# Kernel optimization log

Measured on AMD Instinct MI355X. Metric: run time of the kernel, lower is better.

The kernel has to match this reference:

```python
import jax, jax.numpy as jnp
import numpy as np
from jax import lax

B, C_IN, C_OUT, KK, KS = 8, 32, 64, 4, 3
D, H, W = 32, 64, 64
PAD = 1

def setup_inputs() -> dict:
    key = jax.random.key(0)
    ks = jax.random.split(key, 12)
    s = 0.02
    return {
        "x": jax.random.normal(ks[0], (B, C_IN, D, H, W), jnp.float32),
        # K candidate conv kernels and biases
        "weight": jax.random.normal(ks[1], (KK, C_OUT, C_IN, KS, KS, KS), jnp.float32) * s,
        "cbias": jnp.zeros((KK, C_OUT), jnp.float32),
        "temperature": jnp.float32(34.0),
        # attention key path: BN(affine, eval-mode) -> GELU -> 1x1 conv (linear)
        "bn1_g": jnp.ones((C_IN,), jnp.float32),
        "bn1_b": jnp.zeros((C_IN,), jnp.float32),
        "w1": jax.random.normal(ks[2], (C_IN, C_IN), jnp.float32) * s,
        "b1": jnp.zeros((C_IN,), jnp.float32),
        "bn2_g": jnp.ones((C_IN,), jnp.float32),
        "bn2_b": jnp.zeros((C_IN,), jnp.float32),
        "w2": jax.random.normal(ks[3], (C_IN, C_IN), jnp.float32) * s,
        "b2": jnp.zeros((C_IN,), jnp.float32),
        "bn3_g": jnp.ones((C_IN,), jnp.float32),
        "bn3_b": jnp.zeros((C_IN,), jnp.float32),
        "w3": jax.random.normal(ks[4], (KK, C_IN), jnp.float32) * s,
        "b3": jnp.zeros((KK,), jnp.float32),
    }

def _attention(p, temperature, bn1_g, bn1_b, w1, b1, bn2_g, bn2_b, w2, b2, bn3_g, bn3_b, w3, b3):
    # p: [B, C] pooled features. 1x1x1 convs on 1x1x1 maps == linear layers.
    gelu = lambda t: jax.nn.gelu(t, approximate=False)  # torch nn.GELU default is erf
    a = gelu(p * bn1_g + bn1_b)          # BN (eval: rm=0, rv=1) + GELU
    a = a @ w1.T + b1
    a = gelu(a * bn2_g + bn2_b)
    a = a @ w2.T + b2
    a = a + p                            # ResidualLayer (plain add)
    a = a * bn3_g + bn3_b
    logits = a @ w3.T + b3               # [B, K]
    return jax.nn.softmax(logits / temperature, axis=1)

def reference(x, weight, cbias, temperature, bn1_g, bn1_b, w1, b1,
              bn2_g, bn2_b, w2, b2, bn3_g, bn3_b, w3, b3):
    # x: [B, C_in, D, H, W]
    p = x.mean(axis=(2, 3, 4))  # AdaptiveAvgPool3d(1)
    attn = _attention(p, temperature, bn1_g, bn1_b, w1, b1,
                      bn2_g, bn2_b, w2, b2, bn3_g, bn3_b, w3, b3)  # [B, K]
    # per-sample aggregated kernels / bias
    agg_w = jnp.einsum('bk,koidhw->boidhw', attn, weight)  # [B, O, I, k, k, k]
    agg_b = attn @ cbias                                    # [B, O]
    # grouped-conv trick (groups=B) == per-sample conv3d -> vmap over batch
    def conv1(xi, wi):
        return lax.conv_general_dilated(
            xi[None], wi, window_strides=(1, 1, 1),
            padding=[(PAD, PAD)] * 3,
            dimension_numbers=('NCDHW', 'OIDHW', 'NCDHW'))[0]
    out = jax.vmap(conv1)(x, agg_w)  # [B, O, D, H, W]
    return out + agg_b[:, :, None, None, None]
```

## Files before the change

### kernel.cpp

```cpp
#include <hip/hip_runtime.h>
#include <hip/hip_bf16.h>
#include <math.h>

#define B_   8
#define CIN  32
#define COUT 64
#define KK_  4
#define DD   32
#define HH   64
#define WW   64
#define HW   (HH*WW)
#define DHW  (DD*HH*WW)

typedef __attribute__((ext_vector_type(8)))  short bf16x8;
typedef __attribute__((ext_vector_type(16))) float f32x16;

__device__ __forceinline__ unsigned short f2bf(float f) {
    union { float f; unsigned int u; } v; v.f = f;
    return (unsigned short)((v.u + 0x7FFFu + ((v.u >> 16) & 1u)) >> 16);
}
__device__ __forceinline__ void gll16(const void* g, void* l) {
    __builtin_amdgcn_global_load_lds(
        (const __attribute__((address_space(1))) void*)g,
        (__attribute__((address_space(3))) void*)l, 16, 0, 0);
}

__global__ __launch_bounds__(256) void transpose_kernel(const float* __restrict__ x,
                                                        unsigned short* __restrict__ xt,
                                                        float* __restrict__ pblk) {
    const int t = threadIdx.x;
    const int r = t >> 6, w = t & 63;
    const int hb = blockIdx.x;
    const int h = (hb << 2) + r;
    const int d = blockIdx.y, b = blockIdx.z;

    const float* xb = x + (size_t)b*CIN*DHW + (size_t)d*HW + (size_t)h*WW + w;
    float f[CIN];
    #pragma unroll
    for (int c = 0; c < CIN; ++c) f[c] = xb[(size_t)c * DHW];

    unsigned int packed[CIN/2];
    #pragma unroll
    for (int c2 = 0; c2 < CIN/2; ++c2) {
        unsigned int lo = f2bf(f[2*c2]);
        unsigned int hi = f2bf(f[2*c2+1]);
        packed[c2] = lo | (hi << 16);
    }
    char* row = (char*)xt + (size_t)((b*DD + d)*HH + h) * 4096;
    #pragma unroll
    for (int q = 0; q < 4; ++q) {
        uint4 v = make_uint4(packed[4*q], packed[4*q+1], packed[4*q+2], packed[4*q+3]);
        *(uint4*)(row + q*1024 + (((w << 4)) ^ (q << 4))) = v;
    }

    #pragma unroll
    for (int off = 32; off > 0; off >>= 1) {
        #pragma unroll
        for (int c = 0; c < CIN; ++c) f[c] += __shfl_xor(f[c], off);
    }
    __shared__ float ws4[4][CIN];
    if ((t & 63) < CIN) ws4[r][t & 63] = f[t & 63];
    __syncthreads();
    if (t < CIN)
        pblk[(size_t)((b*DD + d)*16 + hb)*CIN + t] =
            ws4[0][t] + ws4[1][t] + ws4[2][t] + ws4[3][t];
}

__device__ __forceinline__ float gelu_erf(float v) {
    return 0.5f * v * (1.f + erff(v * 0.70710678118654752f));
}

__global__ void attn_kernel(const float* __restrict__ pblk,
                            const float* __restrict__ temperature,
                            const float* __restrict__ bn1_g, const float* __restrict__ bn1_b,
                            const float* __restrict__ w1,    const float* __restrict__ b1,
                            const float* __restrict__ bn2_g, const float* __restrict__ bn2_b,
                            const float* __restrict__ w2,    const float* __restrict__ b2,
                            const float* __restrict__ bn3_g, const float* __restrict__ bn3_b,
                            const float* __restrict__ w3,    const float* __restrict__ b3,
                            const float* __restrict__ cbias,
                            float* __restrict__ attn_out, float* __restrict__ aggb_out) {
    __shared__ float A[B_][CIN], A2[B_][CIN];
    __shared__ float L[B_][KK_], ATT[B_][KK_];
    const int t = threadIdx.x;
    const int b = t >> 5, c = t & 31;

    float pv = 0.f;
    for (int i = 0; i < DD*16; ++i) pv += pblk[(size_t)(b*DD*16 + i)*CIN + c];
    pv *= (1.f / (float)DHW);

    A[b][c] = gelu_erf(pv * bn1_g[c] + bn1_b[c]);
    __syncthreads();

    float s = b1[c];
    for (int j = 0; j < CIN; ++j) s += A[b][j] * w1[c*CIN + j];
    A2[b][c] = gelu_erf(s * bn2_g[c] + bn2_b[c]);
    __syncthreads();

    float s2 = b2[c];
    for (int j = 0; j < CIN; ++j) s2 += A2[b][j] * w2[c*CIN + j];
    s2 += pv;
    s2 = s2 * bn3_g[c] + bn3_b[c];
    __syncthreads();
    A[b][c] = s2;
    __syncthreads();

    if (c < KK_) {
        float lv = b3[c];
        for (int j = 0; j < CIN; ++j) lv += A[b][j] * w3[c*CIN + j];
        L[b][c] = lv;
    }
    __syncthreads();

    const float T = temperature[0];
    if (c < KK_) {
        float m = fmaxf(fmaxf(L[b][0], L[b][1]), fmaxf(L[b][2], L[b][3]));
        float e = expf((L[b][c] - m) / T);
        float den = 0.f;
        for (int j = 0; j < KK_; ++j) den += expf((L[b][j] - m) / T);
        float av = e / den;
        ATT[b][c] = av;
        attn_out[b*KK_ + c] = av;
    }
    __syncthreads();

    for (int o = c; o < COUT; o += CIN) {
        float sb = 0.f;
        for (int k = 0; k < KK_; ++k) sb += ATT[b][k] * cbias[k*COUT + o];
        aggb_out[b*COUT + o] = sb;
    }
}

__global__ void aggw_kernel(const float* __restrict__ weight,
                            const float* __restrict__ attn,
                            unsigned short* __restrict__ wt) {
    const int idx = blockIdx.x * 256 + threadIdx.x;
    const int ci   = idx & 31;
    const int co   = (idx >> 5) & 63;
    int r          = idx >> 11;
    const int kpos = r % 27;
    const int b    = r / 27;
    float s = 0.f;
    #pragma unroll
    for (int k = 0; k < KK_; ++k)
        s += attn[b*KK_ + k] * weight[((k*COUT + co)*CIN + ci)*27 + kpos];
    wt[idx] = f2bf(s);
}

__global__ __launch_bounds__(128, 1) void conv_mfma(const unsigned short* __restrict__ xt,
                                                    const unsigned short* __restrict__ wt,
                                                    const float* __restrict__ aggb,
                                                    float* __restrict__ out) {
    __shared__ char smem[19 * 4096];
    const int t    = threadIdx.x;
    const int lane = t & 63;
    const int wv   = t >> 6;
    const int lw   = lane & 31, lh = lane >> 5;

    const int id = blockIdx.x;
    const int b  = id & 7;
    const int cv = (id >> 3) & 1;
    const int h  = (id >> 4) & 63;
    const int d0 = ((id >> 10) & 7) << 2;

    const char* xb  = (const char*)xt + (size_t)(b*DD)*HH*4096;
    const char* wtb = (const char*)wt + (size_t)b * 27 * 4096 + (cv << 11);

    *(uint4*)&smem[18*4096 + t*32]      = make_uint4(0u,0u,0u,0u);
    *(uint4*)&smem[18*4096 + t*32 + 16] = make_uint4(0u,0u,0u,0u);

    for (int rid = wv; rid < 18; rid += 2) {
        const int j = rid / 3, ho = rid % 3;
        const int zd = d0 - 1 + j, yh = h - 1 + ho;
        char* dst = smem + (size_t)(rid << 12);
        if ((unsigned)zd < DD && (unsigned)yh < HH) {
            const char* src = xb + (size_t)(zd*HH + yh)*4096 + lane*16;
            #pragma unroll
            for (int q = 0; q < 4; ++q) gll16(src + (q << 10), dst + (q << 10));
        } else {
            #pragma unroll
            for (int q = 0; q < 4; ++q)
                *(uint4*)(dst + (q << 10) + lane*16) = make_uint4(0u,0u,0u,0u);
        }
    }

    const int a_off = lw*64 + lh*16;
    bf16x8 avv[27][2];
    #pragma unroll
    for (int kp = 0; kp < 27; ++kp) {
        const char* wk = wtb + (size_t)(kp << 12);
        avv[kp][0] = *(const bf16x8*)(wk + a_off);
        avv[kp][1] = *(const bf16x8*)(wk + 32 + a_off);
    }

    __syncthreads();

    f32x16 acc[4];
    #pragma unroll
    for (int r = 0; r < 4; ++r) acc[r] = (f32x16){};

    const int o0 = lh, o1 = 2 + lh;

    bf16x8 bcp[2][12];
    auto loadB = [&](int p, int par) {
        const int kh = p / 3, kw = p % 3;
        const int wp  = (wv << 5) + lw + kw - 1;
        const bool oob = ((unsigned)wp >= (unsigned)WW);
        const int wpc = oob ? lw : wp;
        const int sw0 = (o0 << 10) + ((wpc << 4) ^ (o0 << 4));
        const int sw1 = (o1 << 10) + ((wpc << 4) ^ (o1 << 4));
        #pragma unroll
        for (int j = 0; j < 6; ++j) {
            const int rb = oob ? 18*4096 : ((j*3 + kh) << 12);
            bcp[par][j*2+0] = *(const bf16x8*)&smem[rb + sw0];
            bcp[par][j*2+1] = *(const bf16x8*)&smem[rb + sw1];
        }
    };

    loadB(0, 0);

    #pragma unroll
    for (int p = 0; p < 9; ++p) {
        const int cur = p & 1, nxt = cur ^ 1;
        if (p < 8) loadB(p + 1, nxt);
        __builtin_amdgcn_sched_barrier(0);
        const int kh = p / 3, kw = p % 3;
        __builtin_amdgcn_s_setprio(1);
        #pragma unroll
        for (int kd = 0; kd < 3; ++kd) {
            const int kp = (kd*3 + kh)*3 + kw;
            #pragma unroll
            for (int r = 0; r < 4; ++r) {
                const int j = r + kd;
                acc[r] = __builtin_amdgcn_mfma_f32_32x32x16_bf16(avv[kp][0], bcp[cur][j*2+0], acc[r], 0, 0, 0);
                acc[r] = __builtin_amdgcn_mfma_f32_32x32x16_bf16(avv[kp][1], bcp[cur][j*2+1], acc[r], 0, 0, 0);
            }
        }
        __builtin_amdgcn_s_setprio(0);
    }

    const float* ab = aggb + b*COUT;
    const int sp0 = h*WW + (wv << 5) + lw;
    #pragma unroll
    for (int reg = 0; reg < 16; ++reg) {
        const int co = (cv << 5) + (reg & 3) + ((reg >> 2) << 3) + (lh << 2);
        const float bb = ab[co];
        float* oc = out + ((size_t)(b*COUT + co))*DHW + sp0;
        #pragma unroll
        for (int r = 0; r < 4; ++r)
            oc[(size_t)(d0 + r)*HW] = acc[r][reg] + bb;
    }
}

extern "C" void kernel_launch(void* const* d_in, const int* in_sizes, int n_in,
                              void* d_out, int out_size, void* d_ws, size_t ws_size,
                              hipStream_t stream) {
    const float* x           = (const float*)d_in[0];
    const float* weight      = (const float*)d_in[1];
    const float* cbias       = (const float*)d_in[2];
    const float* temperature = (const float*)d_in[3];
    const float* bn1_g       = (const float*)d_in[4];
    const float* bn1_b       = (const float*)d_in[5];
    const float* w1          = (const float*)d_in[6];
    const float* b1          = (const float*)d_in[7];
    const float* bn2_g       = (const float*)d_in[8];
    const float* bn2_b       = (const float*)d_in[9];
    const float* w2          = (const float*)d_in[10];
    const float* b2          = (const float*)d_in[11];
    const float* bn3_g       = (const float*)d_in[12];
    const float* bn3_b       = (const float*)d_in[13];
    const float* w3          = (const float*)d_in[14];
    const float* b3          = (const float*)d_in[15];
    float* out = (float*)d_out;

    char* ws = (char*)d_ws;
    float*          attn = (float*)(ws + 1024);
    float*          aggb = (float*)(ws + 4096);
    float*          pblk = (float*)(ws + 65536);
    unsigned short* wt   = (unsigned short*)(ws + 622592);
    unsigned short* xt   = (unsigned short*)(ws + 1507328);

    transpose_kernel<<<dim3(HH/4, DD, B_), 256, 0, stream>>>(x, xt, pblk);
    attn_kernel<<<1, 256, 0, stream>>>(pblk, temperature,
                                       bn1_g, bn1_b, w1, b1,
                                       bn2_g, bn2_b, w2, b2,
                                       bn3_g, bn3_b, w3, b3,
                                       cbias, attn, aggb);
    aggw_kernel<<<(B_*27*COUT*CIN)/256, 256, 0, stream>>>(weight, attn, wt);
    conv_mfma<<<dim3(8192), 128, 0, stream>>>(xt, wt, aggb, out);
}
```

Baseline: 216.5 us.

## Make conv blocks loop over depth with a ring-buffered, prefetched LDS slab pipeline

The conv kernel now launches one 256-thread block per (batch, row), 512 blocks in total. Each block's four waves split the output channels and the width between them, and the block walks all 32 depth planes in steps of four. Input slabs live in a 10-slot LDS ring: the slabs for the next step are prefetched with global_load_lds while the current step runs MFMAs. Weights stay in registers for the whole depth loop, and the bias is folded into the accumulator init. This removes the repeated halo loads and per-block weight reloads of the old 8192-block launch. The cost is less parallelism, and the barrier's vmcnt(63) wait may not guarantee the prefetched slabs have landed before they are read.

```diff
diff --git a/kernel.cpp b/kernel.cpp
--- a/kernel.cpp
+++ b/kernel.cpp
@@ -147,42 +147,24 @@
     wt[idx] = f2bf(s);
 }
 
-__global__ __launch_bounds__(128, 1) void conv_mfma(const unsigned short* __restrict__ xt,
+__global__ __launch_bounds__(256, 1) void conv_mfma(const unsigned short* __restrict__ xt,
                                                     const unsigned short* __restrict__ wt,
                                                     const float* __restrict__ aggb,
                                                     float* __restrict__ out) {
-    __shared__ char smem[19 * 4096];
+    __shared__ char smem[126976];
     const int t    = threadIdx.x;
     const int lane = t & 63;
-    const int wv   = t >> 6;
+    const int wid  = t >> 6;
+    const int cv   = wid >> 1;
+    const int wv   = wid & 1;
     const int lw   = lane & 31, lh = lane >> 5;
 
     const int id = blockIdx.x;
     const int b  = id & 7;
-    const int cv = (id >> 3) & 1;
-    const int h  = (id >> 4) & 63;
-    const int d0 = ((id >> 10) & 7) << 2;
+    const int h  = id >> 3;
 
     const char* xb  = (const char*)xt + (size_t)(b*DD)*HH*4096;
     const char* wtb = (const char*)wt + (size_t)b * 27 * 4096 + (cv << 11);
-
-    *(uint4*)&smem[18*4096 + t*32]      = make_uint4(0u,0u,0u,0u);
-    *(uint4*)&smem[18*4096 + t*32 + 16] = make_uint4(0u,0u,0u,0u);
-
-    for (int rid = wv; rid < 18; rid += 2) {
-        const int j = rid / 3, ho = rid % 3;
-        const int zd = d0 - 1 + j, yh = h - 1 + ho;
-        char* dst = smem + (size_t)(rid << 12);
-        if ((unsigned)zd < DD && (unsigned)yh < HH) {
-            const char* src = xb + (size_t)(zd*HH + yh)*4096 + lane*16;
-            #pragma unroll
-            for (int q = 0; q < 4; ++q) gll16(src + (q << 10), dst + (q << 10));
-        } else {
-            #pragma unroll
-            for (int q = 0; q < 4; ++q)
-                *(uint4*)(dst + (q << 10) + lane*16) = make_uint4(0u,0u,0u,0u);
-        }
-    }
 
     const int a_off = lw*64 + lh*16;
     bf16x8 avv[27][2];
@@ -192,63 +174,108 @@
         avv[kp][0] = *(const bf16x8*)(wk + a_off);
         avv[kp][1] = *(const bf16x8*)(wk + 32 + a_off);
     }
-
+    #pragma unroll
+    for (int kp = 0; kp < 27; ++kp) {
+        asm volatile("" : "+v"(avv[kp][0]));
+        asm volatile("" : "+v"(avv[kp][1]));
+    }
+
+    f32x16 binit;
+    #pragma unroll
+    for (int reg = 0; reg < 16; ++reg)
+        binit[reg] = aggb[b*COUT + (cv << 5) + (reg & 3) + ((reg >> 2) << 3) + (lh << 2)];
+
+    *(uint4*)&smem[122880 + t*16] = make_uint4(0u,0u,0u,0u);
+
+    auto stage_slab = [&](int zd, int slot) {
+        char* sb = smem + slot * 12288;
+        #pragma unroll
+        for (int ho = 0; ho < 3; ++ho) {
+            const int yh = h - 1 + ho;
+            char* dst = sb + (ho << 12);
+            if ((unsigned)zd < DD && (unsigned)yh < HH) {
+                const char* src = xb + ((size_t)(zd*HH + yh) << 12) + lane*16;
+                #pragma unroll
+                for (int q = 0; q < 4; ++q) gll16(src + (q << 10), dst + (q << 10));
+            } else {
+                #pragma unroll
+                for (int q = 0; q < 4; ++q)
+                    *(uint4*)(dst + (q << 10) + lane*16) = make_uint4(0u,0u,0u,0u);
+            }
+        }
+    };
+
+    for (int i = wid; i < 6; i += 4) stage_slab(i - 1, (i + 9) % 10);
     __syncthreads();
 
     f32x16 acc[4];
     #pragma unroll
-    for (int r = 0; r < 4; ++r) acc[r] = (f32x16){};
+    for (int r = 0; r < 4; ++r) acc[r] = binit;
 
     const int o0 = lh, o1 = 2 + lh;
-
+    const int ZR = 122880;
     bf16x8 bcp[2][12];
-    auto loadB = [&](int p, int par) {
-        const int kh = p / 3, kw = p % 3;
-        const int wp  = (wv << 5) + lw + kw - 1;
-        const bool oob = ((unsigned)wp >= (unsigned)WW);
-        const int wpc = oob ? lw : wp;
-        const int sw0 = (o0 << 10) + ((wpc << 4) ^ (o0 << 4));
-        const int sw1 = (o1 << 10) + ((wpc << 4) ^ (o1 << 4));
-        #pragma unroll
-        for (int j = 0; j < 6; ++j) {
-            const int rb = oob ? 18*4096 : ((j*3 + kh) << 12);
-            bcp[par][j*2+0] = *(const bf16x8*)&smem[rb + sw0];
-            bcp[par][j*2+1] = *(const bf16x8*)&smem[rb + sw1];
-        }
-    };
-
-    loadB(0, 0);
-
-    #pragma unroll
-    for (int p = 0; p < 9; ++p) {
-        const int cur = p & 1, nxt = cur ^ 1;
-        if (p < 8) loadB(p + 1, nxt);
-        __builtin_amdgcn_sched_barrier(0);
-        const int kh = p / 3, kw = p % 3;
-        __builtin_amdgcn_s_setprio(1);
-        #pragma unroll
-        for (int kd = 0; kd < 3; ++kd) {
-            const int kp = (kd*3 + kh)*3 + kw;
+
+    for (int s = 0; s < 8; ++s) {
+        const int d0 = s << 2;
+        if (s < 7) {
+            const int zf = d0 + 5 + wid;
+            stage_slab(zf, zf % 10);
+        }
+        int rbj[6];
+        #pragma unroll
+        for (int j = 0; j < 6; ++j) rbj[j] = ((d0 + 9 + j) % 10) * 12288;
+
+        auto loadB = [&](int p, int par) {
+            const int kh = p / 3, kw = p % 3;
+            const int wp  = (wv << 5) + lw + kw - 1;
+            const bool oob = ((unsigned)wp >= (unsigned)WW);
+            const int wpc = oob ? lw : wp;
+            const int sw0 = (o0 << 10) + ((wpc << 4) ^ (o0 << 4));
+            const int sw1 = (o1 << 10) + ((wpc << 4) ^ (o1 << 4));
             #pragma unroll
-            for (int r = 0; r < 4; ++r) {
-                const int j = r + kd;
-                acc[r] = __builtin_amdgcn_mfma_f32_32x32x16_bf16(avv[kp][0], bcp[cur][j*2+0], acc[r], 0, 0, 0);
-                acc[r] = __builtin_amdgcn_mfma_f32_32x32x16_bf16(avv[kp][1], bcp[cur][j*2+1], acc[r], 0, 0, 0);
+            for (int j = 0; j < 6; ++j) {
+                const int base = oob ? ZR : rbj[j] + (kh << 12);
+                bcp[par][j*2+0] = *(const bf16x8*)&smem[base + sw0];
+                bcp[par][j*2+1] = *(const bf16x8*)&smem[base + sw1];
             }
-        }
-        __builtin_amdgcn_s_setprio(0);
-    }
-
-    const float* ab = aggb + b*COUT;
-    const int sp0 = h*WW + (wv << 5) + lw;
-    #pragma unroll
-    for (int reg = 0; reg < 16; ++reg) {
-        const int co = (cv << 5) + (reg & 3) + ((reg >> 2) << 3) + (lh << 2);
-        const float bb = ab[co];
-        float* oc = out + ((size_t)(b*COUT + co))*DHW + sp0;
-        #pragma unroll
-        for (int r = 0; r < 4; ++r)
-            oc[(size_t)(d0 + r)*HW] = acc[r][reg] + bb;
+        };
+
+        loadB(0, 0);
+        #pragma unroll
+        for (int p = 0; p < 9; ++p) {
+            const int cur = p & 1, nxt = cur ^ 1;
+            if (p < 8) loadB(p + 1, nxt);
+            __builtin_amdgcn_sched_barrier(0);
+            const int kh = p / 3, kw = p % 3;
+            #pragma unroll
+            for (int kd = 0; kd < 3; ++kd) {
+                const int kp = (kd*3 + kh)*3 + kw;
+                #pragma unroll
+                for (int r = 0; r < 4; ++r) {
+                    const int j = r + kd;
+                    acc[r] = __builtin_amdgcn_mfma_f32_32x32x16_bf16(avv[kp][0], bcp[cur][j*2+0], acc[r], 0, 0, 0);
+                    acc[r] = __builtin_amdgcn_mfma_f32_32x32x16_bf16(avv[kp][1], bcp[cur][j*2+1], acc[r], 0, 0, 0);
+                }
+            }
+        }
+
+        const int sp0 = h*WW + (wv << 5) + lw;
+        #pragma unroll
+        for (int reg = 0; reg < 16; ++reg) {
+            const int co = (cv << 5) + (reg & 3) + ((reg >> 2) << 3) + (lh << 2);
+            float* oc = out + ((size_t)(b*COUT + co))*DHW + sp0;
+            #pragma unroll
+            for (int r = 0; r < 4; ++r)
+                oc[(size_t)(d0 + r)*HW] = acc[r][reg];
+        }
+        #pragma unroll
+        for (int r = 0; r < 4; ++r) acc[r] = binit;
+
+        if (s < 7) {
+            asm volatile("s_waitcnt vmcnt(63) lgkmcnt(0)" ::: "memory");
+            __builtin_amdgcn_s_barrier();
+        }
     }
 }
 
@@ -287,5 +314,5 @@
                                        bn3_g, bn3_b, w3, b3,
                                        cbias, attn, aggb);
     aggw_kernel<<<(B_*27*COUT*CIN)/256, 256, 0, stream>>>(weight, attn, wt);
-    conv_mfma<<<dim3(8192), 128, 0, stream>>>(xt, wt, aggb, out);
-}
+    conv_mfma<<<dim3(512), 256, 0, stream>>>(xt, wt, aggb, out);
+}
```

Measured after the change: 179.0 us. 17.3% less time.
